# Kernel tuning notes

Measured on AMD Instinct MI355X. Metric: run time of the kernel, lower is better.

## Reference

```python
import jax, jax.numpy as jnp
import numpy as np

B, T, H, QS = 32, 4096, 512, 512

def setup_inputs() -> dict:
    key = jax.random.key(0)
    k1, k2, k3, k4, k5 = jax.random.split(key, 5)
    query = jax.random.normal(k1, (B, 1, QS), dtype=jnp.float32)
    precomputed_key = jax.random.normal(k2, (B, T, H), dtype=jnp.float32)
    value = jax.random.normal(k3, (B, T, H), dtype=jnp.float32)
    mask = jnp.ones((B, T), dtype=bool)  # unused in original forward
    Wq = jax.random.normal(k4, (H, QS), dtype=jnp.float32) * (1.0 / np.sqrt(QS))
    We = jax.random.normal(k5, (H,), dtype=jnp.float32) * (1.0 / np.sqrt(H))
    return {"query": query, "precomputed_key": precomputed_key, "value": value,
            "mask": mask, "Wq": Wq, "We": We}

def reference(query, precomputed_key, value, mask, Wq, We):
    # query_layer: Linear(query_size -> hidden, no bias): x @ Wq.T
    q = jnp.einsum('bqs,hs->bqh', query, Wq)              # [B,1,H]
    # energy: tanh(q + key) then Linear(hidden -> 1, no bias), squeeze
    scores = jnp.einsum('bth,h->bt', jnp.tanh(q + precomputed_key), We)  # [B,T]
    alphas = jax.nn.softmax(scores, axis=1)               # [B,T]
    # bmm(alphas[B,1,T], value[B,T,D]) -> [B,1,D]
    context = jnp.einsum('bt,btd->bd', alphas, value)[:, None, :]
    return context, alphas
```

## Files before the change

kernel.cpp:

```cpp
#include <hip/hip_runtime.h>
#include <math.h>

#define BB 32
#define TT 4096
#define HH 512
#define QQS 512
#define TS 64
#define CH 64

__device__ inline float wave_reduce_sum(float v) {
#pragma unroll
    for (int off = 32; off > 0; off >>= 1) v += __shfl_xor(v, off, 64);
    return v;
}

__device__ inline float wave_reduce_max(float v) {
#pragma unroll
    for (int off = 32; off > 0; off >>= 1) v = fmaxf(v, __shfl_xor(v, off, 64));
    return v;
}

__device__ inline float fast_tanh(float x) {
    x = fminf(fmaxf(x, -15.f), 15.f);
    float e = __expf(-2.f * x);
    return (1.f - e) / (1.f + e);
}

__global__ void qproj_kernel(const float* __restrict__ query,
                             const float* __restrict__ Wq,
                             float* __restrict__ qout) {
    int wid  = (blockIdx.x * blockDim.x + threadIdx.x) >> 6;
    int lane = threadIdx.x & 63;
    int b = wid >> 9;
    int h = wid & (HH - 1);
    const float4* qr = (const float4*)(query + (size_t)b * QQS);
    const float4* wr = (const float4*)(Wq + (size_t)h * QQS);
    float4 a0 = qr[lane],      w0 = wr[lane];
    float4 a1 = qr[lane + 64], w1 = wr[lane + 64];
    float acc = a0.x * w0.x + a0.y * w0.y + a0.z * w0.z + a0.w * w0.w
              + a1.x * w1.x + a1.y * w1.y + a1.z * w1.z + a1.w * w1.w;
    acc = wave_reduce_sum(acc);
    if (lane == 0) qout[wid] = acc;
}

__global__ __launch_bounds__(256) void fused_kernel(
        const float* __restrict__ key, const float* __restrict__ value,
        const float* __restrict__ qb,  const float* __restrict__ We,
        float* __restrict__ scores, float* __restrict__ mbuf,
        float* __restrict__ zbuf,   float* __restrict__ part) {
    __shared__ float q_l[HH];
    __shared__ float w_l[HH];
    __shared__ float s_lds[CH];
    __shared__ float e_lds[CH];
    __shared__ float ctx_lds[HH];

    int b = blockIdx.x / TS, c = blockIdx.x % TS;
    int tid = threadIdx.x;
    q_l[tid]       = qb[(size_t)b * HH + tid];
    q_l[tid + 256] = qb[(size_t)b * HH + tid + 256];
    w_l[tid]       = We[tid];
    w_l[tid + 256] = We[tid + 256];
    __syncthreads();

    int w = tid >> 6, lane = tid & 63;
    size_t row0 = (size_t)b * TT + (size_t)c * CH;

    for (int rr = 0; rr < CH / 4; ++rr) {
        int r = rr * 4 + w;
        const float4* kr = (const float4*)(key + (row0 + r) * HH);
        float4 k0 = kr[lane];
        float4 k1 = kr[lane + 64];
        int h0 = lane * 4, h1 = 256 + lane * 4;
        float p = 0.f;
        p += fast_tanh(q_l[h0 + 0] + k0.x) * w_l[h0 + 0];
        p += fast_tanh(q_l[h0 + 1] + k0.y) * w_l[h0 + 1];
        p += fast_tanh(q_l[h0 + 2] + k0.z) * w_l[h0 + 2];
        p += fast_tanh(q_l[h0 + 3] + k0.w) * w_l[h0 + 3];
        p += fast_tanh(q_l[h1 + 0] + k1.x) * w_l[h1 + 0];
        p += fast_tanh(q_l[h1 + 1] + k1.y) * w_l[h1 + 1];
        p += fast_tanh(q_l[h1 + 2] + k1.z) * w_l[h1 + 2];
        p += fast_tanh(q_l[h1 + 3] + k1.w) * w_l[h1 + 3];
        p = wave_reduce_sum(p);
        if (lane == 0) s_lds[r] = p;
    }
    __syncthreads();

    if (w == 0) {
        float s = s_lds[lane];
        float m = wave_reduce_max(s);
        float e = __expf(s - m);
        e_lds[lane] = e;
        float z = wave_reduce_sum(e);
        if (lane == 0) {
            mbuf[b * TS + c] = m;
            zbuf[b * TS + c] = z;
        }
    } else if (w == 1 && lane < CH / 4) {
        ((float4*)(scores + row0))[lane] = ((float4*)s_lds)[lane];
    }
    __syncthreads();

    int d4 = tid & 127, rg = tid >> 7;
    const float4* vp = (const float4*)(value + row0 * HH);
    float4 acc = make_float4(0.f, 0.f, 0.f, 0.f);
#pragma unroll 4
    for (int r = rg; r < CH; r += 2) {
        float a = e_lds[r];
        float4 v = vp[(size_t)r * (HH / 4) + d4];
        acc.x += a * v.x; acc.y += a * v.y; acc.z += a * v.z; acc.w += a * v.w;
    }
    if (rg == 0) ((float4*)ctx_lds)[d4] = acc;
    __syncthreads();
    if (rg == 1) {
        float4 t = ((float4*)ctx_lds)[d4];
        t.x += acc.x; t.y += acc.y; t.z += acc.z; t.w += acc.w;
        ((float4*)(part + ((size_t)c * BB + b) * HH))[d4] = t;
    }
}

__global__ void finalize_kernel(const float* __restrict__ scores,
                                const float* __restrict__ mbuf,
                                const float* __restrict__ zbuf,
                                const float* __restrict__ part,
                                float* __restrict__ alphas,
                                float* __restrict__ ctx) {
    int tid = threadIdx.x, lane = tid & 63;
    if (blockIdx.x < BB) {
        int b = blockIdx.x;
        float m_l = mbuf[b * TS + lane];
        float z_l = zbuf[b * TS + lane];
        float M = wave_reduce_max(m_l);
        float Z = wave_reduce_sum(__expf(m_l - M) * z_l);
        float invZ = 1.f / Z;
        const float4* sp = (const float4*)(scores + (size_t)b * TT);
        float4* ap = (float4*)(alphas + (size_t)b * TT);
#pragma unroll
        for (int i = 0; i < 4; ++i) {
            float4 s = sp[tid + i * 256];
            float4 a;
            a.x = __expf(s.x - M) * invZ;
            a.y = __expf(s.y - M) * invZ;
            a.z = __expf(s.z - M) * invZ;
            a.w = __expf(s.w - M) * invZ;
            ap[tid + i * 256] = a;
        }
    } else {
        int i = blockIdx.x - BB;
        int b = i >> 1;
        int d = (i & 1) * 256 + tid;
        __shared__ float scale[TS];
        if (tid < TS) {
            float m_l = mbuf[b * TS + lane];
            float z_l = zbuf[b * TS + lane];
            float M = wave_reduce_max(m_l);
            float Z = wave_reduce_sum(__expf(m_l - M) * z_l);
            scale[lane] = __expf(m_l - M) / Z;
        }
        __syncthreads();
        float s = 0.f;
#pragma unroll
        for (int c2 = 0; c2 < TS; ++c2)
            s += scale[c2] * part[((size_t)c2 * BB + b) * HH + d];
        ctx[(size_t)b * HH + d] = s;
    }
}

extern "C" void kernel_launch(void* const* d_in, const int* in_sizes, int n_in,
                              void* d_out, int out_size, void* d_ws, size_t ws_size,
                              hipStream_t stream) {
    const float* query = (const float*)d_in[0];
    const float* key   = (const float*)d_in[1];
    const float* value = (const float*)d_in[2];
    const float* Wq    = (const float*)d_in[4];
    const float* We    = (const float*)d_in[5];

    float* ctx    = (float*)d_out;
    float* alphas = (float*)d_out + BB * HH;

    float* qbuf   = (float*)d_ws;
    float* sc     = qbuf + BB * HH;
    float* mbuf   = sc + BB * TT;
    float* zbuf   = mbuf + BB * TS;
    float* part   = zbuf + BB * TS;

    qproj_kernel<<<(BB * HH) / 4, 256, 0, stream>>>(query, Wq, qbuf);
    fused_kernel<<<BB * TS, 256, 0, stream>>>(key, value, qbuf, We, sc, mbuf, zbuf, part);
    finalize_kernel<<<BB + 2 * BB, 256, 0, stream>>>(sc, mbuf, zbuf, part, alphas, ctx);
}
```

Before: 109.0 us.

## Use exp2/rcp tanh, register-resident q/We, two-row scoring, and store unnormalized alphas

Rewrites tanh as 1 - 2/(exp2(k*2log2e + q')+1), using the hardware exp2 and rcp builtins with q pre-scaled, and keeps the q/We slices in registers instead of LDS. Each wave now scores two rows per iteration and does a half-wave reduction. The fused kernel writes the local exp values straight into the alphas output, so finalize only rescales them per chunk instead of re-reading scores and recomputing exp. It also changes the value accumulation order to contiguous rows per group. The risks are approximate rcp/exp precision and the missing clamp for large inputs.

Result: no change. 109.1 us (+0.1%).

```diff
diff --git a/kernel.cpp b/kernel.cpp
--- a/kernel.cpp
+++ b/kernel.cpp
@@ -8,6 +8,23 @@
 #define TS 64
 #define CH 64
 
+#define TANH_K 2.8853900817779268f
+
+__device__ inline float fast_exp2(float x) {
+#if __has_builtin(__builtin_amdgcn_exp2f)
+    return __builtin_amdgcn_exp2f(x);
+#else
+    return __expf(x * 0.6931471805599453f);
+#endif
+}
+__device__ inline float fast_rcp(float x) {
+#if __has_builtin(__builtin_amdgcn_rcpf)
+    return __builtin_amdgcn_rcpf(x);
+#else
+    return 1.f / x;
+#endif
+}
+
 __device__ inline float wave_reduce_sum(float v) {
 #pragma unroll
     for (int off = 32; off > 0; off >>= 1) v += __shfl_xor(v, off, 64);
@@ -18,12 +35,6 @@
 #pragma unroll
     for (int off = 32; off > 0; off >>= 1) v = fmaxf(v, __shfl_xor(v, off, 64));
     return v;
-}
-
-__device__ inline float fast_tanh(float x) {
-    x = fminf(fmaxf(x, -15.f), 15.f);
-    float e = __expf(-2.f * x);
-    return (1.f - e) / (1.f + e);
 }
 
 __global__ void qproj_kernel(const float* __restrict__ query,
@@ -43,45 +54,64 @@
     if (lane == 0) qout[wid] = acc;
 }
 
+__device__ inline float tanh_term(float k, float qc, float w, float p) {
+    float e = fast_exp2(fmaf(k, TANH_K, qc));
+    float r = fast_rcp(e + 1.f);
+    float th = fmaf(-2.f, r, 1.f);
+    return fmaf(th, w, p);
+}
+
 __global__ __launch_bounds__(256) void fused_kernel(
         const float* __restrict__ key, const float* __restrict__ value,
         const float* __restrict__ qb,  const float* __restrict__ We,
-        float* __restrict__ scores, float* __restrict__ mbuf,
+        float* __restrict__ alphas, float* __restrict__ mbuf,
         float* __restrict__ zbuf,   float* __restrict__ part) {
-    __shared__ float q_l[HH];
-    __shared__ float w_l[HH];
     __shared__ float s_lds[CH];
     __shared__ float e_lds[CH];
     __shared__ float ctx_lds[HH];
 
     int b = blockIdx.x / TS, c = blockIdx.x % TS;
     int tid = threadIdx.x;
-    q_l[tid]       = qb[(size_t)b * HH + tid];
-    q_l[tid + 256] = qb[(size_t)b * HH + tid + 256];
-    w_l[tid]       = We[tid];
-    w_l[tid + 256] = We[tid + 256];
-    __syncthreads();
-
     int w = tid >> 6, lane = tid & 63;
     size_t row0 = (size_t)b * TT + (size_t)c * CH;
 
-    for (int rr = 0; rr < CH / 4; ++rr) {
-        int r = rr * 4 + w;
-        const float4* kr = (const float4*)(key + (row0 + r) * HH);
-        float4 k0 = kr[lane];
-        float4 k1 = kr[lane + 64];
-        int h0 = lane * 4, h1 = 256 + lane * 4;
-        float p = 0.f;
-        p += fast_tanh(q_l[h0 + 0] + k0.x) * w_l[h0 + 0];
-        p += fast_tanh(q_l[h0 + 1] + k0.y) * w_l[h0 + 1];
-        p += fast_tanh(q_l[h0 + 2] + k0.z) * w_l[h0 + 2];
-        p += fast_tanh(q_l[h0 + 3] + k0.w) * w_l[h0 + 3];
-        p += fast_tanh(q_l[h1 + 0] + k1.x) * w_l[h1 + 0];
-        p += fast_tanh(q_l[h1 + 1] + k1.y) * w_l[h1 + 1];
-        p += fast_tanh(q_l[h1 + 2] + k1.z) * w_l[h1 + 2];
-        p += fast_tanh(q_l[h1 + 3] + k1.w) * w_l[h1 + 3];
-        p = wave_reduce_sum(p);
-        if (lane == 0) s_lds[r] = p;
+    const float4* qv = (const float4*)(qb + (size_t)b * HH);
+    const float4* wv = (const float4*)We;
+    float4 q0 = qv[lane], q1 = qv[lane + 64];
+    float4 w0 = wv[lane], w1 = wv[lane + 64];
+    q0.x *= TANH_K; q0.y *= TANH_K; q0.z *= TANH_K; q0.w *= TANH_K;
+    q1.x *= TANH_K; q1.y *= TANH_K; q1.z *= TANH_K; q1.w *= TANH_K;
+
+#pragma unroll 2
+    for (int rr = 0; rr < CH / 8; ++rr) {
+        int r0 = rr * 8 + w, r1 = r0 + 4;
+        const float4* k0p = (const float4*)(key + (row0 + r0) * HH);
+        const float4* k1p = (const float4*)(key + (row0 + r1) * HH);
+        float4 ka = k0p[lane], kb = k0p[lane + 64];
+        float4 kc = k1p[lane], kd = k1p[lane + 64];
+        float p0 = 0.f, p1 = 0.f;
+        p0 = tanh_term(ka.x, q0.x, w0.x, p0);
+        p0 = tanh_term(ka.y, q0.y, w0.y, p0);
+        p0 = tanh_term(ka.z, q0.z, w0.z, p0);
+        p0 = tanh_term(ka.w, q0.w, w0.w, p0);
+        p0 = tanh_term(kb.x, q1.x, w1.x, p0);
+        p0 = tanh_term(kb.y, q1.y, w1.y, p0);
+        p0 = tanh_term(kb.z, q1.z, w1.z, p0);
+        p0 = tanh_term(kb.w, q1.w, w1.w, p0);
+        p1 = tanh_term(kc.x, q0.x, w0.x, p1);
+        p1 = tanh_term(kc.y, q0.y, w0.y, p1);
+        p1 = tanh_term(kc.z, q0.z, w0.z, p1);
+        p1 = tanh_term(kc.w, q0.w, w0.w, p1);
+        p1 = tanh_term(kd.x, q1.x, w1.x, p1);
+        p1 = tanh_term(kd.y, q1.y, w1.y, p1);
+        p1 = tanh_term(kd.z, q1.z, w1.z, p1);
+        p1 = tanh_term(kd.w, q1.w, w1.w, p1);
+        float a0 = __shfl_xor(p0, 32, 64);
+        float a1 = __shfl_xor(p1, 32, 64);
+        float ws = (lane < 32) ? (p0 + a0) : (p1 + a1);
+#pragma unroll
+        for (int off = 16; off > 0; off >>= 1) ws += __shfl_xor(ws, off, 64);
+        if ((lane & 31) == 0) s_lds[(lane < 32) ? r0 : r1] = ws;
     }
     __syncthreads();
 
@@ -90,13 +120,12 @@
         float m = wave_reduce_max(s);
         float e = __expf(s - m);
         e_lds[lane] = e;
+        alphas[row0 + lane] = e;
         float z = wave_reduce_sum(e);
         if (lane == 0) {
             mbuf[b * TS + c] = m;
             zbuf[b * TS + c] = z;
         }
-    } else if (w == 1 && lane < CH / 4) {
-        ((float4*)(scores + row0))[lane] = ((float4*)s_lds)[lane];
     }
     __syncthreads();
 
@@ -104,7 +133,7 @@
     const float4* vp = (const float4*)(value + row0 * HH);
     float4 acc = make_float4(0.f, 0.f, 0.f, 0.f);
 #pragma unroll 4
-    for (int r = rg; r < CH; r += 2) {
+    for (int r = rg * 32; r < rg * 32 + 32; ++r) {
         float a = e_lds[r];
         float4 v = vp[(size_t)r * (HH / 4) + d4];
         acc.x += a * v.x; acc.y += a * v.y; acc.z += a * v.z; acc.w += a * v.w;
@@ -118,13 +147,13 @@
     }
 }
 
-__global__ void finalize_kernel(const float* __restrict__ scores,
-                                const float* __restrict__ mbuf,
+__global__ void finalize_kernel(const float* __restrict__ mbuf,
                                 const float* __restrict__ zbuf,
                                 const float* __restrict__ part,
                                 float* __restrict__ alphas,
                                 float* __restrict__ ctx) {
     int tid = threadIdx.x, lane = tid & 63;
+    __shared__ float scale[TS];
     if (blockIdx.x < BB) {
         int b = blockIdx.x;
         float m_l = mbuf[b * TS + lane];
@@ -132,30 +161,26 @@
         float M = wave_reduce_max(m_l);
         float Z = wave_reduce_sum(__expf(m_l - M) * z_l);
         float invZ = 1.f / Z;
-        const float4* sp = (const float4*)(scores + (size_t)b * TT);
+        if (tid < TS) scale[tid] = __expf(m_l - M) * invZ;
+        __syncthreads();
         float4* ap = (float4*)(alphas + (size_t)b * TT);
 #pragma unroll
         for (int i = 0; i < 4; ++i) {
-            float4 s = sp[tid + i * 256];
-            float4 a;
-            a.x = __expf(s.x - M) * invZ;
-            a.y = __expf(s.y - M) * invZ;
-            a.z = __expf(s.z - M) * invZ;
-            a.w = __expf(s.w - M) * invZ;
-            ap[tid + i * 256] = a;
+            int idx = tid + i * 256;
+            float4 a = ap[idx];
+            float s = scale[idx >> 4];
+            a.x *= s; a.y *= s; a.z *= s; a.w *= s;
+            ap[idx] = a;
         }
     } else {
         int i = blockIdx.x - BB;
         int b = i >> 1;
         int d = (i & 1) * 256 + tid;
-        __shared__ float scale[TS];
-        if (tid < TS) {
-            float m_l = mbuf[b * TS + lane];
-            float z_l = zbuf[b * TS + lane];
-            float M = wave_reduce_max(m_l);
-            float Z = wave_reduce_sum(__expf(m_l - M) * z_l);
-            scale[lane] = __expf(m_l - M) / Z;
-        }
+        float m_l = mbuf[b * TS + lane];
+        float z_l = zbuf[b * TS + lane];
+        float M = wave_reduce_max(m_l);
+        float Z = wave_reduce_sum(__expf(m_l - M) * z_l);
+        if (tid < TS) scale[tid] = __expf(m_l - M) / Z;
         __syncthreads();
         float s = 0.f;
 #pragma unroll
@@ -178,12 +203,11 @@
     float* alphas = (float*)d_out + BB * HH;
 
     float* qbuf   = (float*)d_ws;
-    float* sc     = qbuf + BB * HH;
-    float* mbuf   = sc + BB * TT;
+    float* mbuf   = qbuf + BB * HH;
     float* zbuf   = mbuf + BB * TS;
     float* part   = zbuf + BB * TS;
 
     qproj_kernel<<<(BB * HH) / 4, 256, 0, stream>>>(query, Wq, qbuf);
-    fused_kernel<<<BB * TS, 256, 0, stream>>>(key, value, qbuf, We, sc, mbuf, zbuf, part);
-    finalize_kernel<<<BB + 2 * BB, 256, 0, stream>>>(sc, mbuf, zbuf, part, alphas, ctx);
-}
+    fused_kernel<<<BB * TS, 256, 0, stream>>>(key, value, qbuf, We, alphas, mbuf, zbuf, part);
+    finalize_kernel<<<BB + 2 * BB, 256, 0, stream>>>(mbuf, zbuf, part, alphas, ctx);
+}
```
